# Performance work log

Hardware: AMD Instinct MI355X
Metric: run time of the kernel (lower is better)

Reference implementation:

```python
import jax, jax.numpy as jnp
import numpy as np

N_NODES = 100000
N_EDGES = 3200000
IN_FEAT = 128


def gcn_conv(x, src, dst, W, b, num_nodes):
    # PyG GCNConv: h = x @ W, then symmetric-normalized aggregation with self-loops.
    h = x @ W  # [N, out]
    # add self loops
    loop = jnp.arange(num_nodes, dtype=src.dtype)
    s = jnp.concatenate([src, loop])
    d = jnp.concatenate([dst, loop])
    # degree over destination (col) with unit edge weights
    deg = jax.ops.segment_sum(jnp.ones_like(s, dtype=h.dtype), d, num_segments=num_nodes)
    dinv = jnp.where(deg > 0, jax.lax.rsqrt(deg), 0.0)
    norm = dinv[s] * dinv[d]  # [E+N]
    msg = norm[:, None] * h[s]  # gather source features, scale per edge
    out = jax.ops.segment_sum(msg, d, num_segments=num_nodes)
    return out + b


def setup_inputs() -> dict:
    key = jax.random.key(0)
    ks = jax.random.split(key, 8)
    x = jax.random.normal(ks[0], (N_NODES, IN_FEAT), dtype=jnp.float32)
    edge_index = jax.random.randint(ks[1], (2, N_EDGES), 0, N_NODES, dtype=jnp.int64)
    def glorot(k, shape):
        lim = np.sqrt(6.0 / (shape[0] + shape[1]))
        return jax.random.uniform(k, shape, jnp.float32, -lim, lim)
    return {
        "x": x,
        "edge_index": edge_index,
        "W1": glorot(ks[2], (IN_FEAT, 4)), "b1": jnp.zeros((4,), jnp.float32),
        "W2": glorot(ks[3], (4, 2)),       "b2": jnp.zeros((2,), jnp.float32),
        "W3": glorot(ks[4], (2, 1)),       "b3": jnp.zeros((1,), jnp.float32),
    }


def reference(x, edge_index, W1, b1, W2, b2, W3, b3):
    src, dst = edge_index[0], edge_index[1]
    n = x.shape[0]
    h = gcn_conv(x, src, dst, W1, b1, n)
    h = jax.nn.relu(h)
    # F.dropout(training=self.training): inference mode -> identity
    h = gcn_conv(h, src, dst, W2, b2, n)
    h = jax.nn.relu(h)
    h = gcn_conv(h, src, dst, W3, b3, n)
    return jax.nn.sigmoid(h)  # [N, 1]
```

## Files before the change

### kernel.cpp

```cpp
#include <hip/hip_runtime.h>
#include <math.h>


#define TPB 256
#define CHUNK 4096
#define EPT (CHUNK / TPB)
#define SLAB2 9216
#define NSMAX 1024

__global__ __launch_bounds__(TPB) void k_part(
    const int* __restrict__ src, const int* __restrict__ dst,
    unsigned int* __restrict__ slab, int* __restrict__ lstartT,
    int NB, int NBP, int NS, int E)
{
    __shared__ int hist[512];
    __shared__ unsigned int sorted[CHUNK];
    __shared__ int wtot[4];
    int t = threadIdx.x;
    int base = blockIdx.x * CHUNK;
    int n = min(CHUNK, E - base);
    hist[t] = 0; hist[t + 256] = 0;
    __syncthreads();
    unsigned int meta[EPT];
#pragma unroll
    for (int k = 0; k < EPT; ++k) {
        int li = k * TPB + t;
        if (li < n) {
            int d = dst[base + li];
            int lp = atomicAdd(&hist[d >> 8], 1);
            meta[k] = ((unsigned)d << 13) | (unsigned)lp;
        } else meta[k] = 0xFFFFFFFFu;
    }
    __syncthreads();
    int v0 = hist[2 * t], v1 = hist[2 * t + 1];
    int pr = v0 + v1;
    int x = pr;
    int lane = t & 63;
    for (int d = 1; d < 64; d <<= 1) {
        int y = __shfl_up(x, d);
        if (lane >= d) x += y;
    }
    if (lane == 63) wtot[t >> 6] = x;
    __syncthreads();
    int w = t >> 6;
    int woff = 0;
#pragma unroll
    for (int i = 0; i < 4; ++i) if (i < w) woff += wtot[i];
    int excl = woff + x - pr;
    hist[2 * t] = excl;
    hist[2 * t + 1] = excl + v0;
    __syncthreads();
#pragma unroll
    for (int k = 0; k < EPT; ++k) {
        if (meta[k] != 0xFFFFFFFFu) {
            unsigned m = meta[k];
            int d = (int)(m >> 13);
            int lp = (int)(m & 0x1FFFu);
            unsigned p = (unsigned)src[base + k * TPB + t] | ((unsigned)(d & 255) << 17);
            sorted[hist[d >> 8] + lp] = p;
        }
    }
    __syncthreads();
    const uint4* s4 = (const uint4*)sorted;
    uint4* g4 = (uint4*)(slab + (size_t)base);
    for (int i = t; i < CHUNK / 4; i += TPB) g4[i] = s4[i];
    for (int i = t; i < NBP; i += TPB)
        lstartT[(size_t)i * NS + blockIdx.x] = (i < NB) ? hist[i] : n;
}

__global__ __launch_bounds__(TPB) void k_degree(
    const unsigned int* __restrict__ slab, const int* __restrict__ lstartT,
    int* __restrict__ ssrc, int* __restrict__ cnt, int* __restrict__ off,
    float* __restrict__ dinv, int NS, int NB, int N)
{
    __shared__ unsigned int pl[SLAB2];
    __shared__ int slen[NSMAX];
    __shared__ int c[TPB];
    __shared__ int cur[TPB];
    __shared__ int wtot[4];
    int t = threadIdx.x, b = blockIdx.x;
    c[t] = 0;
    int stv[NSMAX / TPB], lenv[NSMAX / TPB];
#pragma unroll
    for (int ci = 0; ci < NSMAX / TPB; ++ci) {
        int j = ci * TPB + t;
        int st = 0, len = 0;
        if (j < NS) {
            st  = lstartT[(size_t)b * NS + j];
            len = lstartT[(size_t)(b + 1) * NS + j] - st;
        }
        stv[ci] = st; lenv[ci] = len;
        slen[j] = len;
    }
    __syncthreads();
    int lane = t & 63, w = t >> 6;
    int s0 = slen[4*t], s1 = slen[4*t+1], s2 = slen[4*t+2], s3 = slen[4*t+3];
    int pq = s0 + s1 + s2 + s3, xs = pq;
    for (int d = 1; d < 64; d <<= 1) { int y = __shfl_up(xs, d); if (lane >= d) xs += y; }
    if (lane == 63) wtot[w] = xs;
    __syncthreads();
    int woff = 0;
#pragma unroll
    for (int i = 0; i < 4; ++i) if (i < w) woff += wtot[i];
    int e0 = woff + xs - pq;
    slen[4*t]   = e0;
    slen[4*t+1] = e0 + s0;
    slen[4*t+2] = e0 + s0 + s1;
    slen[4*t+3] = e0 + s0 + s1 + s2;
    __syncthreads();
#pragma unroll
    for (int ci = 0; ci < NSMAX / TPB; ++ci) {
        int j = ci * TPB + t;
        if (j < NS && lenv[ci] > 0) {
            int lo = slen[j];
            const unsigned int* sp = slab + (size_t)j * CHUNK + stv[ci];
            for (int k = 0; k < lenv[ci]; ++k) {
                if (lo + k >= SLAB2) break;
                pl[lo + k] = sp[k];
            }
        }
    }
    __syncthreads();
    int total = 0;
    {
        total = min(slen[NSMAX - 1], SLAB2);
    }
    for (int i = t; i < total; i += TPB) atomicAdd(&c[(pl[i] >> 17) & 255], 1);
    __syncthreads();
    int cv = c[t];
    int xc = cv;
    for (int d = 1; d < 64; d <<= 1) { int y = __shfl_up(xc, d); if (lane >= d) xc += y; }
    if (lane == 63) wtot[w] = xc;
    __syncthreads();
    int woff2 = 0;
#pragma unroll
    for (int i = 0; i < 4; ++i) if (i < w) woff2 += wtot[i];
    int excl = woff2 + xc - cv;
    int v = (b << 8) + t;
    if (v < N) {
        cnt[v] = cv;
        off[v] = b * SLAB2 + excl;
        dinv[v] = rsqrtf((float)(cv + 1));
    }
    cur[t] = excl;
    __syncthreads();
    int* sb = ssrc + (size_t)b * SLAB2;
    for (int i = t; i < total; i += TPB) {
        unsigned p = pl[i];
        int pos = atomicAdd(&cur[(p >> 17) & 255], 1);
        sb[pos] = (int)(p & 0x1FFFFu);
    }
}

__global__ __launch_bounds__(TPB) void k_node1(
    const float* __restrict__ x, const float* __restrict__ W1,
    const float* __restrict__ dinv, float* __restrict__ hs1, int n) {
    __shared__ float Ws[512];
    for (int i = threadIdx.x; i < 512; i += TPB) Ws[i] = W1[i];
    __syncthreads();
    int t = blockIdx.x * TPB + threadIdx.x;
    int v = t >> 2, p = t & 3;
    if (v >= n) return;
    const float4* xr = (const float4*)(x + (size_t)v * 128);
    float a0 = 0.f, a1 = 0.f, a2 = 0.f, a3 = 0.f;
#pragma unroll
    for (int i = 0; i < 8; ++i) {
        int c = p + i * 4;
        float4 xx = xr[c];
        const float* w = &Ws[c * 16];
        a0 += xx.x * w[0] + xx.y * w[4] + xx.z * w[8]  + xx.w * w[12];
        a1 += xx.x * w[1] + xx.y * w[5] + xx.z * w[9]  + xx.w * w[13];
        a2 += xx.x * w[2] + xx.y * w[6] + xx.z * w[10] + xx.w * w[14];
        a3 += xx.x * w[3] + xx.y * w[7] + xx.z * w[11] + xx.w * w[15];
    }
    a0 += __shfl_xor(a0, 1); a0 += __shfl_xor(a0, 2);
    a1 += __shfl_xor(a1, 1); a1 += __shfl_xor(a1, 2);
    a2 += __shfl_xor(a2, 1); a2 += __shfl_xor(a2, 2);
    a3 += __shfl_xor(a3, 1); a3 += __shfl_xor(a3, 2);
    if (p == 0) {
        float di = dinv[v];
        ((float4*)hs1)[v] = make_float4(di * a0, di * a1, di * a2, di * a3);
    }
}

__global__ __launch_bounds__(TPB) void k_gather1(
    const int* __restrict__ off, const int* __restrict__ cnt,
    const int* __restrict__ ssrc, const float* __restrict__ hs1,
    const float* __restrict__ dinv, const float* __restrict__ b1,
    const float* __restrict__ W2, float* __restrict__ hs2, int n) {
    int t = blockIdx.x * TPB + threadIdx.x;
    int v = t >> 3, p = t & 7;
    if (v >= n) return;
    int base = off[v], c = cnt[v];
    float4 acc = make_float4(0.f, 0.f, 0.f, 0.f);
    for (int i = p; i < c; i += 8) {
        int s = ssrc[base + i];
        float4 h = ((const float4*)hs1)[s];
        acc.x += h.x; acc.y += h.y; acc.z += h.z; acc.w += h.w;
    }
    acc.x += __shfl_xor(acc.x, 1); acc.x += __shfl_xor(acc.x, 2); acc.x += __shfl_xor(acc.x, 4);
    acc.y += __shfl_xor(acc.y, 1); acc.y += __shfl_xor(acc.y, 2); acc.y += __shfl_xor(acc.y, 4);
    acc.z += __shfl_xor(acc.z, 1); acc.z += __shfl_xor(acc.z, 2); acc.z += __shfl_xor(acc.z, 4);
    acc.w += __shfl_xor(acc.w, 1); acc.w += __shfl_xor(acc.w, 2); acc.w += __shfl_xor(acc.w, 4);
    if (p == 0) {
        float4 hv = ((const float4*)hs1)[v];
        float di = dinv[v];
        float o0 = fmaxf(di * (acc.x + hv.x) + b1[0], 0.f);
        float o1 = fmaxf(di * (acc.y + hv.y) + b1[1], 0.f);
        float o2 = fmaxf(di * (acc.z + hv.z) + b1[2], 0.f);
        float o3 = fmaxf(di * (acc.w + hv.w) + b1[3], 0.f);
        float h0 = o0 * W2[0] + o1 * W2[2] + o2 * W2[4] + o3 * W2[6];
        float h1 = o0 * W2[1] + o1 * W2[3] + o2 * W2[5] + o3 * W2[7];
        ((float2*)hs2)[v] = make_float2(di * h0, di * h1);
    }
}

__global__ __launch_bounds__(TPB) void k_gather2(
    const int* __restrict__ off, const int* __restrict__ cnt,
    const int* __restrict__ ssrc, const float* __restrict__ hs2,
    const float* __restrict__ dinv, const float* __restrict__ b2,
    const float* __restrict__ W3, float* __restrict__ hs3, int n) {
    int t = blockIdx.x * TPB + threadIdx.x;
    int v = t >> 3, p = t & 7;
    if (v >= n) return;
    int base = off[v], c = cnt[v];
    float2 acc = make_float2(0.f, 0.f);
    for (int i = p; i < c; i += 8) {
        int s = ssrc[base + i];
        float2 h = ((const float2*)hs2)[s];
        acc.x += h.x; acc.y += h.y;
    }
    acc.x += __shfl_xor(acc.x, 1); acc.x += __shfl_xor(acc.x, 2); acc.x += __shfl_xor(acc.x, 4);
    acc.y += __shfl_xor(acc.y, 1); acc.y += __shfl_xor(acc.y, 2); acc.y += __shfl_xor(acc.y, 4);
    if (p == 0) {
        float2 hv = ((const float2*)hs2)[v];
        float di = dinv[v];
        float o0 = fmaxf(di * (acc.x + hv.x) + b2[0], 0.f);
        float o1 = fmaxf(di * (acc.y + hv.y) + b2[1], 0.f);
        float h3 = o0 * W3[0] + o1 * W3[1];
        hs3[v] = di * h3;
    }
}

__global__ __launch_bounds__(TPB) void k_gather3(
    const int* __restrict__ off, const int* __restrict__ cnt,
    const int* __restrict__ ssrc, const float* __restrict__ hs3,
    const float* __restrict__ dinv, const float* __restrict__ b3,
    float* __restrict__ out, int n) {
    int t = blockIdx.x * TPB + threadIdx.x;
    int v = t >> 3, p = t & 7;
    if (v >= n) return;
    int base = off[v], c = cnt[v];
    float acc = 0.f;
    for (int i = p; i < c; i += 8) acc += hs3[ssrc[base + i]];
    acc += __shfl_xor(acc, 1); acc += __shfl_xor(acc, 2); acc += __shfl_xor(acc, 4);
    if (p == 0) {
        float di = dinv[v];
        float agg = di * (acc + hs3[v]) + b3[0];
        out[v] = 1.0f / (1.0f + __expf(-agg));
    }
}

extern "C" void kernel_launch(void* const* d_in, const int* in_sizes, int n_in,
                              void* d_out, int out_size, void* d_ws, size_t ws_size,
                              hipStream_t stream) {
    const float* x  = (const float*)d_in[0];
    const int* ei   = (const int*)d_in[1];
    const float* W1 = (const float*)d_in[2];
    const float* b1 = (const float*)d_in[3];
    const float* W2 = (const float*)d_in[4];
    const float* b2 = (const float*)d_in[5];
    const float* W3 = (const float*)d_in[6];
    const float* b3 = (const float*)d_in[7];
    float* out = (float*)d_out;

    const int N = in_sizes[0] / 128;
    const int E = in_sizes[1] / 2;
    const int* src = ei;
    const int* dst = ei + E;

    const int NS  = (E + CHUNK - 1) / CHUNK;
    const int NB  = (N + 255) >> 8;
    const int NBP = NB + 1;

    char* w = (char*)d_ws;
    auto carve = [&](size_t bytes) { char* p = w; w += (bytes + 15) & ~(size_t)15; return p; };
    unsigned int* slab = (unsigned int*)carve((size_t)NS * CHUNK * 4);
    int* lstartT       = (int*)carve((size_t)NBP * NS * 4);
    int* ssrc          = (int*)carve((size_t)NB * SLAB2 * 4);
    int* cnt           = (int*)carve((size_t)N * 4);
    int* off           = (int*)carve((size_t)N * 4);
    float* dinv        = (float*)carve((size_t)N * 4);
    float* hs1 = (float*)slab;
    float* hs2 = hs1 + (size_t)4 * N;
    float* hs3 = hs2 + (size_t)2 * N;

    const int nbN4 = (4 * N + TPB - 1) / TPB;
    const int nbN8 = (8 * N + TPB - 1) / TPB;

    k_part   <<<NS, TPB, 0, stream>>>(src, dst, slab, lstartT, NB, NBP, NS, E);
    k_degree <<<NB, TPB, 0, stream>>>(slab, lstartT, ssrc, cnt, off, dinv, NS, NB, N);
    k_node1  <<<nbN4, TPB, 0, stream>>>(x, W1, dinv, hs1, N);
    k_gather1<<<nbN8, TPB, 0, stream>>>(off, cnt, ssrc, hs1, dinv, b1, W2, hs2, N);
    k_gather2<<<nbN8, TPB, 0, stream>>>(off, cnt, ssrc, hs2, dinv, b2, W3, hs3, N);
    k_gather3<<<nbN8, TPB, 0, stream>>>(off, cnt, ssrc, hs3, dinv, b3, out, N);
}
```

Measured before the change: 214.9 us.

## Fuse x@W1 projection into partition kernel and unroll gather loops by four

The node projection x@W1 now runs in extra blocks of the edge-partition kernel, which removes a separate launch and lets the dense projection overlap the edge bucketing. The dinv scaling is applied in the degree kernel, which writes the scaled hs1 buffer. The three gather kernels issue four independent index loads and feature loads per iteration to raise memory-level parallelism. This adds an intermediate h1 buffer and extra writes, and hs2/hs3 still alias the slab buffer.

```diff
diff --git a/kernel.cpp b/kernel.cpp
--- a/kernel.cpp
+++ b/kernel.cpp
@@ -11,12 +11,42 @@
 __global__ __launch_bounds__(TPB) void k_part(
     const int* __restrict__ src, const int* __restrict__ dst,
     unsigned int* __restrict__ slab, int* __restrict__ lstartT,
-    int NB, int NBP, int NS, int E)
+    const float* __restrict__ x, const float* __restrict__ W1,
+    float* __restrict__ h1,
+    int NB, int NBP, int NS, int E, int N)
 {
     __shared__ int hist[512];
     __shared__ unsigned int sorted[CHUNK];
     __shared__ int wtot[4];
     int t = threadIdx.x;
+
+    if (blockIdx.x >= NS) {
+        float* Ws = (float*)sorted;
+        for (int i = t; i < 512; i += TPB) Ws[i] = W1[i];
+        __syncthreads();
+        int tt = (blockIdx.x - NS) * TPB + t;
+        int v = tt >> 2, p = tt & 3;
+        if (v >= N) return;
+        const float4* xr = (const float4*)(x + (size_t)v * 128);
+        float a0 = 0.f, a1 = 0.f, a2 = 0.f, a3 = 0.f;
+#pragma unroll
+        for (int i = 0; i < 8; ++i) {
+            int cc = p + i * 4;
+            float4 xx = xr[cc];
+            const float* wv = &Ws[cc * 16];
+            a0 += xx.x*wv[0] + xx.y*wv[4] + xx.z*wv[8]  + xx.w*wv[12];
+            a1 += xx.x*wv[1] + xx.y*wv[5] + xx.z*wv[9]  + xx.w*wv[13];
+            a2 += xx.x*wv[2] + xx.y*wv[6] + xx.z*wv[10] + xx.w*wv[14];
+            a3 += xx.x*wv[3] + xx.y*wv[7] + xx.z*wv[11] + xx.w*wv[15];
+        }
+        a0 += __shfl_xor(a0,1); a0 += __shfl_xor(a0,2);
+        a1 += __shfl_xor(a1,1); a1 += __shfl_xor(a1,2);
+        a2 += __shfl_xor(a2,1); a2 += __shfl_xor(a2,2);
+        a3 += __shfl_xor(a3,1); a3 += __shfl_xor(a3,2);
+        if (p == 0) ((float4*)h1)[v] = make_float4(a0, a1, a2, a3);
+        return;
+    }
+
     int base = blockIdx.x * CHUNK;
     int n = min(CHUNK, E - base);
     hist[t] = 0; hist[t + 256] = 0;
@@ -34,19 +64,19 @@
     __syncthreads();
     int v0 = hist[2 * t], v1 = hist[2 * t + 1];
     int pr = v0 + v1;
-    int x = pr;
+    int xsc = pr;
     int lane = t & 63;
     for (int d = 1; d < 64; d <<= 1) {
-        int y = __shfl_up(x, d);
-        if (lane >= d) x += y;
-    }
-    if (lane == 63) wtot[t >> 6] = x;
+        int y = __shfl_up(xsc, d);
+        if (lane >= d) xsc += y;
+    }
+    if (lane == 63) wtot[t >> 6] = xsc;
     __syncthreads();
     int w = t >> 6;
     int woff = 0;
 #pragma unroll
     for (int i = 0; i < 4; ++i) if (i < w) woff += wtot[i];
-    int excl = woff + x - pr;
+    int excl = woff + xsc - pr;
     hist[2 * t] = excl;
     hist[2 * t + 1] = excl + v0;
     __syncthreads();
@@ -71,7 +101,8 @@
 __global__ __launch_bounds__(TPB) void k_degree(
     const unsigned int* __restrict__ slab, const int* __restrict__ lstartT,
     int* __restrict__ ssrc, int* __restrict__ cnt, int* __restrict__ off,
-    float* __restrict__ dinv, int NS, int NB, int N)
+    float* __restrict__ dinv, const float* __restrict__ h1, float* __restrict__ hs1,
+    int NS, int NB, int N)
 {
     __shared__ unsigned int pl[SLAB2];
     __shared__ int slen[NSMAX];
@@ -121,10 +152,7 @@
         }
     }
     __syncthreads();
-    int total = 0;
-    {
-        total = min(slen[NSMAX - 1], SLAB2);
-    }
+    int total = min(slen[NSMAX - 1], SLAB2);
     for (int i = t; i < total; i += TPB) atomicAdd(&c[(pl[i] >> 17) & 255], 1);
     __syncthreads();
     int cv = c[t];
@@ -140,7 +168,10 @@
     if (v < N) {
         cnt[v] = cv;
         off[v] = b * SLAB2 + excl;
-        dinv[v] = rsqrtf((float)(cv + 1));
+        float di = rsqrtf((float)(cv + 1));
+        dinv[v] = di;
+        float4 hv = ((const float4*)h1)[v];
+        ((float4*)hs1)[v] = make_float4(di*hv.x, di*hv.y, di*hv.z, di*hv.w);
     }
     cur[t] = excl;
     __syncthreads();
@@ -149,37 +180,6 @@
         unsigned p = pl[i];
         int pos = atomicAdd(&cur[(p >> 17) & 255], 1);
         sb[pos] = (int)(p & 0x1FFFFu);
-    }
-}
-
-__global__ __launch_bounds__(TPB) void k_node1(
-    const float* __restrict__ x, const float* __restrict__ W1,
-    const float* __restrict__ dinv, float* __restrict__ hs1, int n) {
-    __shared__ float Ws[512];
-    for (int i = threadIdx.x; i < 512; i += TPB) Ws[i] = W1[i];
-    __syncthreads();
-    int t = blockIdx.x * TPB + threadIdx.x;
-    int v = t >> 2, p = t & 3;
-    if (v >= n) return;
-    const float4* xr = (const float4*)(x + (size_t)v * 128);
-    float a0 = 0.f, a1 = 0.f, a2 = 0.f, a3 = 0.f;
-#pragma unroll
-    for (int i = 0; i < 8; ++i) {
-        int c = p + i * 4;
-        float4 xx = xr[c];
-        const float* w = &Ws[c * 16];
-        a0 += xx.x * w[0] + xx.y * w[4] + xx.z * w[8]  + xx.w * w[12];
-        a1 += xx.x * w[1] + xx.y * w[5] + xx.z * w[9]  + xx.w * w[13];
-        a2 += xx.x * w[2] + xx.y * w[6] + xx.z * w[10] + xx.w * w[14];
-        a3 += xx.x * w[3] + xx.y * w[7] + xx.z * w[11] + xx.w * w[15];
-    }
-    a0 += __shfl_xor(a0, 1); a0 += __shfl_xor(a0, 2);
-    a1 += __shfl_xor(a1, 1); a1 += __shfl_xor(a1, 2);
-    a2 += __shfl_xor(a2, 1); a2 += __shfl_xor(a2, 2);
-    a3 += __shfl_xor(a3, 1); a3 += __shfl_xor(a3, 2);
-    if (p == 0) {
-        float di = dinv[v];
-        ((float4*)hs1)[v] = make_float4(di * a0, di * a1, di * a2, di * a3);
     }
 }
 
@@ -192,18 +192,26 @@
     int v = t >> 3, p = t & 7;
     if (v >= n) return;
     int base = off[v], c = cnt[v];
+    const float4* H = (const float4*)hs1;
     float4 acc = make_float4(0.f, 0.f, 0.f, 0.f);
-    for (int i = p; i < c; i += 8) {
-        int s = ssrc[base + i];
-        float4 h = ((const float4*)hs1)[s];
-        acc.x += h.x; acc.y += h.y; acc.z += h.z; acc.w += h.w;
+    for (int i = p; i < c; i += 32) {
+        bool m1 = (i + 8 < c), m2 = (i + 16 < c), m3 = (i + 24 < c);
+        int s0 = ssrc[base + i];
+        int s1 = ssrc[base + (m1 ? i + 8  : i)];
+        int s2 = ssrc[base + (m2 ? i + 16 : i)];
+        int s3 = ssrc[base + (m3 ? i + 24 : i)];
+        float4 h0 = H[s0], h1v = H[s1], h2 = H[s2], h3 = H[s3];
+        acc.x += h0.x; acc.y += h0.y; acc.z += h0.z; acc.w += h0.w;
+        if (m1) { acc.x += h1v.x; acc.y += h1v.y; acc.z += h1v.z; acc.w += h1v.w; }
+        if (m2) { acc.x += h2.x;  acc.y += h2.y;  acc.z += h2.z;  acc.w += h2.w; }
+        if (m3) { acc.x += h3.x;  acc.y += h3.y;  acc.z += h3.z;  acc.w += h3.w; }
     }
     acc.x += __shfl_xor(acc.x, 1); acc.x += __shfl_xor(acc.x, 2); acc.x += __shfl_xor(acc.x, 4);
     acc.y += __shfl_xor(acc.y, 1); acc.y += __shfl_xor(acc.y, 2); acc.y += __shfl_xor(acc.y, 4);
     acc.z += __shfl_xor(acc.z, 1); acc.z += __shfl_xor(acc.z, 2); acc.z += __shfl_xor(acc.z, 4);
     acc.w += __shfl_xor(acc.w, 1); acc.w += __shfl_xor(acc.w, 2); acc.w += __shfl_xor(acc.w, 4);
     if (p == 0) {
-        float4 hv = ((const float4*)hs1)[v];
+        float4 hv = H[v];
         float di = dinv[v];
         float o0 = fmaxf(di * (acc.x + hv.x) + b1[0], 0.f);
         float o1 = fmaxf(di * (acc.y + hv.y) + b1[1], 0.f);
@@ -224,16 +232,24 @@
     int v = t >> 3, p = t & 7;
     if (v >= n) return;
     int base = off[v], c = cnt[v];
+    const float2* H = (const float2*)hs2;
     float2 acc = make_float2(0.f, 0.f);
-    for (int i = p; i < c; i += 8) {
-        int s = ssrc[base + i];
-        float2 h = ((const float2*)hs2)[s];
-        acc.x += h.x; acc.y += h.y;
+    for (int i = p; i < c; i += 32) {
+        bool m1 = (i + 8 < c), m2 = (i + 16 < c), m3 = (i + 24 < c);
+        int s0 = ssrc[base + i];
+        int s1 = ssrc[base + (m1 ? i + 8  : i)];
+        int s2 = ssrc[base + (m2 ? i + 16 : i)];
+        int s3 = ssrc[base + (m3 ? i + 24 : i)];
+        float2 h0 = H[s0], h1 = H[s1], h2 = H[s2], h3 = H[s3];
+        acc.x += h0.x; acc.y += h0.y;
+        if (m1) { acc.x += h1.x; acc.y += h1.y; }
+        if (m2) { acc.x += h2.x; acc.y += h2.y; }
+        if (m3) { acc.x += h3.x; acc.y += h3.y; }
     }
     acc.x += __shfl_xor(acc.x, 1); acc.x += __shfl_xor(acc.x, 2); acc.x += __shfl_xor(acc.x, 4);
     acc.y += __shfl_xor(acc.y, 1); acc.y += __shfl_xor(acc.y, 2); acc.y += __shfl_xor(acc.y, 4);
     if (p == 0) {
-        float2 hv = ((const float2*)hs2)[v];
+        float2 hv = H[v];
         float di = dinv[v];
         float o0 = fmaxf(di * (acc.x + hv.x) + b2[0], 0.f);
         float o1 = fmaxf(di * (acc.y + hv.y) + b2[1], 0.f);
@@ -252,7 +268,18 @@
     if (v >= n) return;
     int base = off[v], c = cnt[v];
     float acc = 0.f;
-    for (int i = p; i < c; i += 8) acc += hs3[ssrc[base + i]];
+    for (int i = p; i < c; i += 32) {
+        bool m1 = (i + 8 < c), m2 = (i + 16 < c), m3 = (i + 24 < c);
+        int s0 = ssrc[base + i];
+        int s1 = ssrc[base + (m1 ? i + 8  : i)];
+        int s2 = ssrc[base + (m2 ? i + 16 : i)];
+        int s3 = ssrc[base + (m3 ? i + 24 : i)];
+        float h0 = hs3[s0], h1 = hs3[s1], h2 = hs3[s2], h3 = hs3[s3];
+        acc += h0;
+        if (m1) acc += h1;
+        if (m2) acc += h2;
+        if (m3) acc += h3;
+    }
     acc += __shfl_xor(acc, 1); acc += __shfl_xor(acc, 2); acc += __shfl_xor(acc, 4);
     if (p == 0) {
         float di = dinv[v];
@@ -291,16 +318,16 @@
     int* cnt           = (int*)carve((size_t)N * 4);
     int* off           = (int*)carve((size_t)N * 4);
     float* dinv        = (float*)carve((size_t)N * 4);
-    float* hs1 = (float*)slab;
-    float* hs2 = hs1 + (size_t)4 * N;
+    float* h1          = (float*)carve((size_t)4 * N * 4);
+    float* hs1         = (float*)carve((size_t)4 * N * 4);
+    float* hs2 = (float*)slab;
     float* hs3 = hs2 + (size_t)2 * N;
 
-    const int nbN4 = (4 * N + TPB - 1) / TPB;
+    const int nb1  = (4 * N + TPB - 1) / TPB;
     const int nbN8 = (8 * N + TPB - 1) / TPB;
 
-    k_part   <<<NS, TPB, 0, stream>>>(src, dst, slab, lstartT, NB, NBP, NS, E);
-    k_degree <<<NB, TPB, 0, stream>>>(slab, lstartT, ssrc, cnt, off, dinv, NS, NB, N);
-    k_node1  <<<nbN4, TPB, 0, stream>>>(x, W1, dinv, hs1, N);
+    k_part   <<<NS + nb1, TPB, 0, stream>>>(src, dst, slab, lstartT, x, W1, h1, NB, NBP, NS, E, N);
+    k_degree <<<NB, TPB, 0, stream>>>(slab, lstartT, ssrc, cnt, off, dinv, h1, hs1, NS, NB, N);
     k_gather1<<<nbN8, TPB, 0, stream>>>(off, cnt, ssrc, hs1, dinv, b1, W2, hs2, N);
     k_gather2<<<nbN8, TPB, 0, stream>>>(off, cnt, ssrc, hs2, dinv, b2, W3, hs3, N);
     k_gather3<<<nbN8, TPB, 0, stream>>>(off, cnt, ssrc, hs3, dinv, b3, out, N);
```

Result: no change. 214.0 us (-0.4%).
